# Kernel optimization log

Measured on AMD Instinct MI355X. Metric: run time of the kernel, lower is better.

The kernel has to match this reference:

```python
import jax, jax.numpy as jnp
import numpy as np

N_NODES = 50000
N_EDGES = 800000
DIM = 128
HEADS = 8
DK = DIM // HEADS  # 16
SQRT_DK = float(np.sqrt(DK))


def setup_inputs() -> dict:
    key = jax.random.key(0)
    ks = jax.random.split(key, 12)
    inp = {
        "h": jax.random.normal(ks[0], (N_NODES, DIM), jnp.float32),
        "src": jax.random.randint(ks[1], (N_EDGES,), 0, N_NODES, jnp.int32),
        "dst": jax.random.randint(ks[2], (N_EDGES,), 0, N_NODES, jnp.int32),
        "Wk": jax.random.normal(ks[3], (DIM, DIM), jnp.float32) / np.sqrt(DIM),
        "bk": jnp.zeros((DIM,), jnp.float32),
        "Wq": jax.random.normal(ks[4], (DIM, DIM), jnp.float32) / np.sqrt(DIM),
        "bq": jnp.zeros((DIM,), jnp.float32),
        "Wv": jax.random.normal(ks[5], (DIM, DIM), jnp.float32) / np.sqrt(DIM),
        "bv": jnp.zeros((DIM,), jnp.float32),
        "Wa": jax.random.normal(ks[6], (DIM, DIM), jnp.float32) / np.sqrt(DIM),
        "ba": jnp.zeros((DIM,), jnp.float32),
        "rel_att": jax.random.normal(ks[7], (HEADS, DK, DK), jnp.float32) / np.sqrt(DK),
        "rel_msg": jax.random.normal(ks[8], (HEADS, DK, DK), jnp.float32) / np.sqrt(DK),
        "rel_pri": jnp.ones((HEADS,), jnp.float32),
        "skip": jnp.ones((1,), jnp.float32),
    }
    return inp


def reference(h, src, dst, Wk, bk, Wq, bq, Wv, bv, Wa, ba, rel_att, rel_msg, rel_pri, skip):
    N = h.shape[0]
    # node-level projections -> [N, H, d_k]
    k = (h @ Wk + bk).reshape(N, HEADS, DK)
    q = (h @ Wq + bq).reshape(N, HEADS, DK)
    v = (h @ Wv + bv).reshape(N, HEADS, DK)
    # relation-specific transforms
    k = jnp.einsum('nhi,hij->nhj', k, rel_att)
    v = jnp.einsum('nhi,hij->nhj', v, rel_msg)
    # per-edge score: dot(q[dst], k[src]) over d_k -> [E, H]
    score = jnp.einsum('ehd,ehd->eh', q[dst], k[src]) * rel_pri / SQRT_DK
    # segment softmax over destination nodes (edge_softmax, norm_by='dst')
    smax = jax.ops.segment_max(score, dst, num_segments=N)  # [N, H]
    e = jnp.exp(score - smax[dst])
    ssum = jax.ops.segment_sum(e, dst, num_segments=N)  # [N, H]
    attn = e / ssum[dst]  # [E, H]
    # weighted scatter-sum of messages: sum_e v[src_e] * attn_e -> [N, H, d_k]
    m = v[src] * attn[:, :, None]
    t = jax.ops.segment_sum(m, dst, num_segments=N).reshape(N, DIM)
    # target-specific aggregation (dropout in eval mode = identity, use_norm=False)
    trans_out = t @ Wa + ba
    alpha = jax.nn.sigmoid(skip)  # [1], broadcasts
    new_h = trans_out * alpha + h * (1.0 - alpha)
    return new_h
```

## Files before the change

### kernel.cpp

```cpp
#include <hip/hip_runtime.h>
#include <stdint.h>

#define NN 50000
#define NE 800000

typedef __bf16 v8bf __attribute__((ext_vector_type(8)));
typedef float  v4f  __attribute__((ext_vector_type(4)));
typedef unsigned short v8us __attribute__((ext_vector_type(8)));

#define EXP2F(x) __builtin_amdgcn_exp2f(x)

__device__ __forceinline__ float bf2f(unsigned short u) {
    return __uint_as_float(((unsigned)u) << 16);
}
__device__ __forceinline__ unsigned short f2bf(float f) {
    unsigned u = __float_as_uint(f);
    u += 0x7FFFu + ((u >> 16) & 1u);
    return (unsigned short)(u >> 16);
}
__device__ __forceinline__ float ldf(const void* p, size_t i, int isb) {
    return isb ? bf2f(((const unsigned short*)p)[i]) : ((const float*)p)[i];
}

__global__ __launch_bounds__(128) void k_prep(
    const void* __restrict__ Wq, const void* __restrict__ bq,
    const void* __restrict__ Wk, const void* __restrict__ bk,
    const void* __restrict__ Wv, const void* __restrict__ bv,
    const void* __restrict__ Wa, const void* __restrict__ ba,
    const void* __restrict__ rel_att, const void* __restrict__ rel_msg,
    const void* __restrict__ rel_pri, const int* __restrict__ dst,
    unsigned* __restrict__ CNTP,
    int* __restrict__ FLAG, unsigned short* __restrict__ WTb,
    float* __restrict__ BC)
{
    int b = blockIdx.x;
    int j = threadIdx.x;
    if (b >= 512) {
        int e = (b - 512) * 128 + j;
        atomicAdd(&CNTP[(unsigned)dst[e] << 4], 1u);
        return;
    }
    const unsigned rp0 = ((const unsigned*)rel_pri)[0];
    const int isb = ((rp0 & 0xFFFFu) != 0u) ? 1 : 0;
    int m = b >> 7;
    int i = b & 127;
    if (b == 0 && j == 0) FLAG[0] = isb;
    if (m == 0) {
        WTb[((size_t)(0 * 128 + j)) * 128 + i] = f2bf(ldf(Wq, i * 128 + j, isb));
        if (i == 0) BC[j] = ldf(bq, j, isb);
    } else if (m == 3) {
        WTb[((size_t)(3 * 128 + j)) * 128 + i] = f2bf(ldf(Wa, i * 128 + j, isb));
        if (i == 0) BC[3 * 128 + j] = ldf(ba, j, isb);
    } else {
        const void* W    = (m == 1) ? Wk : Wv;
        const void* bias = (m == 1) ? bk : bv;
        const void* R    = (m == 1) ? rel_att : rel_msg;
        int hh = j >> 4, jj = j & 15;
        float scale = (m == 1) ? ldf(rel_pri, hh, isb) * 0.25f : 1.0f;
        float acc = 0.f, bacc = 0.f;
        #pragma unroll
        for (int l = 0; l < 16; ++l) {
            float r = ldf(R, hh * 256 + l * 16 + jj, isb);
            acc  += ldf(W, i * 128 + hh * 16 + l, isb) * r;
            bacc += ldf(bias, hh * 16 + l, isb) * r;
        }
        WTb[((size_t)(m * 128 + j)) * 128 + i] = f2bf(acc * scale);
        if (i == 0) BC[m * 128 + j] = bacc * scale;
    }
}

#define NSB 98
__global__ __launch_bounds__(256) void k_qkvscan(
    const void* __restrict__ h, const unsigned short* __restrict__ WTb,
    const float* __restrict__ BC, const int* __restrict__ FLAG,
    unsigned short* __restrict__ Qb, unsigned short* __restrict__ KVb,
    const unsigned* __restrict__ CNTP, unsigned* __restrict__ CURP,
    unsigned* __restrict__ RPS, unsigned* __restrict__ BSUM,
    unsigned* __restrict__ BOFF, unsigned* __restrict__ DONE)
{
    __shared__ __align__(16) unsigned short Ah[64][136];
    __shared__ __align__(16) unsigned short Bh[128][136];
    __shared__ int lastFlag;
    const int tid = threadIdx.x;

    if (blockIdx.x >= 782) {
        unsigned* shs = (unsigned*)&Ah[0][0];
        int sb = blockIdx.x - 782;
        int g0 = sb * 512 + tid * 2, g1 = g0 + 1;
        unsigned v0 = (g0 < NN) ? CNTP[(size_t)g0 << 4] : 0u;
        unsigned v1 = (g1 < NN) ? CNTP[(size_t)g1 << 4] : 0u;
        if (g0 < NN) CURP[(size_t)g0 << 4] = 0u;
        if (g1 < NN) CURP[(size_t)g1 << 4] = 0u;
        unsigned pv = v0 + v1;
        shs[tid] = pv;
        __syncthreads();
        #pragma unroll
        for (int off = 1; off < 256; off <<= 1) {
            unsigned t = 0;
            if (tid >= off) t = shs[tid - off];
            __syncthreads();
            if (tid >= off) shs[tid] += t;
            __syncthreads();
        }
        unsigned excl = shs[tid] - pv;
        if (g0 < NN) RPS[g0] = excl;
        if (g1 < NN) RPS[g1] = excl + v0;
        if (tid == 255) atomicExch(&BSUM[sb], shs[255]);
        __syncthreads();
        if (tid == 0) {
            __threadfence();
            lastFlag = (atomicAdd(DONE, 1u) == NSB - 1);
        }
        __syncthreads();
        if (!lastFlag) return;
        unsigned bv = (tid < NSB) ? atomicAdd(&BSUM[tid], 0u) : 0u;
        __syncthreads();
        shs[tid] = bv;
        __syncthreads();
        #pragma unroll
        for (int off = 1; off < 256; off <<= 1) {
            unsigned t = 0;
            if (tid >= off) t = shs[tid - off];
            __syncthreads();
            if (tid >= off) shs[tid] += t;
            __syncthreads();
        }
        if (tid < NSB) BOFF[tid] = shs[tid] - bv;
        return;
    }

    const int isb = FLAG[0];
    const int rowBase = blockIdx.x * 64;

    if (isb) {
        #pragma unroll
        for (int i = 0; i < 4; ++i) {
            int lin = tid + i * 256;
            int row = lin >> 4, kc = (lin & 15) * 8;
            int gr = rowBase + row;
            uint4 u = make_uint4(0, 0, 0, 0);
            if (gr < NN) u = *(const uint4*)((const unsigned short*)h + (size_t)gr * 128 + kc);
            *(uint4*)&Ah[row][kc] = u;
        }
    } else {
        #pragma unroll
        for (int i = 0; i < 8; ++i) {
            int lin = tid + i * 256;
            int row = lin >> 5, c4 = (lin & 31) * 4;
            int gr = rowBase + row;
            ushort4 o = make_ushort4(0, 0, 0, 0);
            if (gr < NN) {
                float4 f = *(const float4*)((const float*)h + (size_t)gr * 128 + c4);
                o.x = f2bf(f.x); o.y = f2bf(f.y); o.z = f2bf(f.z); o.w = f2bf(f.w);
            }
            *(ushort4*)&Ah[row][c4] = o;
        }
    }

    const int w = tid >> 6, l = tid & 63;
    const int lr = l & 15, q = l >> 4;
    v4f accK[8];

    for (int m = 0; m < 3; ++m) {
        if (m) __syncthreads();
        #pragma unroll
        for (int i = 0; i < 8; ++i) {
            int lin = tid + i * 256;
            int col = lin >> 4, kc = (lin & 15) * 8;
            uint4 u = *(const uint4*)(WTb + ((size_t)(m * 128 + col)) * 128 + kc);
            *(uint4*)&Bh[col][kc] = u;
        }
        __syncthreads();

        v4f acc[8];
        #pragma unroll
        for (int nt = 0; nt < 8; ++nt) {
            float bj = BC[m * 128 + nt * 16 + lr];
            acc[nt] = (v4f){bj, bj, bj, bj};
        }
        #pragma unroll
        for (int kk = 0; kk < 4; ++kk) {
            v8bf a = *(const v8bf*)&Ah[w * 16 + lr][kk * 32 + q * 8];
            #pragma unroll
            for (int nt = 0; nt < 8; ++nt) {
                v8bf b = *(const v8bf*)&Bh[nt * 16 + lr][kk * 32 + q * 8];
                acc[nt] = __builtin_amdgcn_mfma_f32_16x16x32_bf16(a, b, acc[nt], 0, 0, 0);
            }
        }
        if (m == 0) {
            #pragma unroll
            for (int nt = 0; nt < 8; ++nt)
                #pragma unroll
                for (int r = 0; r < 4; ++r) {
                    int row = rowBase + w * 16 + q * 4 + r;
                    if (row < NN)
                        Qb[(size_t)row * 128 + nt * 16 + lr] = f2bf(acc[nt][r]);
                }
        } else if (m == 1) {
            #pragma unroll
            for (int nt = 0; nt < 8; ++nt) accK[nt] = acc[nt];
        } else {
            #pragma unroll
            for (int nt = 0; nt < 8; ++nt)
                #pragma unroll
                for (int r = 0; r < 4; ++r) {
                    int row = rowBase + w * 16 + q * 4 + r;
                    if (row < NN) {
                        ushort2 kv;
                        kv.x = f2bf(accK[nt][r]);
                        kv.y = f2bf(acc[nt][r]);
                        *(ushort2*)&KVb[(size_t)row * 256 + (nt * 16 + lr) * 2] = kv;
                    }
                }
        }
    }
}

__global__ __launch_bounds__(256) void k_fill(
    const int* __restrict__ src, const int* __restrict__ dst,
    const unsigned* __restrict__ RPS, const unsigned* __restrict__ BOFF,
    unsigned* __restrict__ CURP, int* __restrict__ ESRC)
{
    int t = blockIdx.x * 256 + threadIdx.x;
    if (t >= NE / 4) return;
    int e = t * 4;
    const int4 d4 = *(const int4*)(dst + e);
    const int4 s4 = *(const int4*)(src + e);
    unsigned p0 = atomicAdd(&CURP[(size_t)(unsigned)d4.x << 4], 1u);
    unsigned p1 = atomicAdd(&CURP[(size_t)(unsigned)d4.y << 4], 1u);
    unsigned p2 = atomicAdd(&CURP[(size_t)(unsigned)d4.z << 4], 1u);
    unsigned p3 = atomicAdd(&CURP[(size_t)(unsigned)d4.w << 4], 1u);
    ESRC[(int)(RPS[d4.x] + BOFF[d4.x >> 9] + p0)] = s4.x;
    ESRC[(int)(RPS[d4.y] + BOFF[d4.y >> 9] + p1)] = s4.y;
    ESRC[(int)(RPS[d4.z] + BOFF[d4.z >> 9] + p2)] = s4.z;
    ESRC[(int)(RPS[d4.w] + BOFF[d4.w >> 9] + p3)] = s4.w;
}

__global__ __launch_bounds__(256) void k_attn(
    const unsigned* __restrict__ RPS, const unsigned* __restrict__ BOFF,
    const int* __restrict__ ESRC,
    const unsigned short* __restrict__ Qb, const unsigned short* __restrict__ KVb,
    unsigned short* __restrict__ Tb)
{
    int d = (blockIdx.x * 256 + threadIdx.x) >> 6;
    int lane = threadIdx.x & 63;
    int hl = lane >> 5;
    int sub = lane & 31;
    int beg = (int)(RPS[d] + BOFF[d >> 9]);
    int end = (d == NN - 1) ? NE : (int)(RPS[d + 1] + BOFF[(d + 1) >> 9]);
    const float LOG2E = 1.4426950408889634f;

    const ushort4 qu = *(const ushort4*)(Qb + (size_t)d * 128 + sub * 4);
    float q0 = bf2f(qu.x) * LOG2E, q1 = bf2f(qu.y) * LOG2E;
    float q2 = bf2f(qu.z) * LOG2E, q3 = bf2f(qu.w) * LOG2E;

    float s = 0.f, o0 = 0.f, o1 = 0.f, o2 = 0.f, o3 = 0.f;
    v8us kvA[4]; int vA[4];
    if (beg < end) {
        #pragma unroll
        for (int t = 0; t < 4; ++t) {
            int idx = beg + 2 * t + hl;
            vA[t] = idx < end;
            int sid = ESRC[vA[t] ? idx : end - 1];
            kvA[t] = *(const v8us*)(KVb + (size_t)sid * 256 + sub * 8);
        }
    }
    for (int j = beg; j < end; j += 8) {
        v8us kvB[4]; int vB[4] = {0, 0, 0, 0};
        int jn = j + 8;
        if (jn < end) {
            #pragma unroll
            for (int t = 0; t < 4; ++t) {
                int idx = jn + 2 * t + hl;
                vB[t] = idx < end;
                int sid = ESRC[vB[t] ? idx : end - 1];
                kvB[t] = *(const v8us*)(KVb + (size_t)sid * 256 + sub * 8);
            }
        }
        #pragma unroll
        for (int t = 0; t < 4; ++t) {
            float p = q0 * bf2f(kvA[t][0]) + q1 * bf2f(kvA[t][2])
                    + q2 * bf2f(kvA[t][4]) + q3 * bf2f(kvA[t][6]);
            p += __shfl_xor(p, 1);
            p += __shfl_xor(p, 2);
            float w = vA[t] ? EXP2F(p) : 0.f;
            s  += w;
            o0 += w * bf2f(kvA[t][1]);
            o1 += w * bf2f(kvA[t][3]);
            o2 += w * bf2f(kvA[t][5]);
            o3 += w * bf2f(kvA[t][7]);
        }
        #pragma unroll
        for (int t = 0; t < 4; ++t) { kvA[t] = kvB[t]; vA[t] = vB[t]; }
    }
    s  += __shfl_xor(s, 32);
    o0 += __shfl_xor(o0, 32);
    o1 += __shfl_xor(o1, 32);
    o2 += __shfl_xor(o2, 32);
    o3 += __shfl_xor(o3, 32);
    float r = (s > 0.f) ? (1.0f / s) : 0.f;
    if (hl == 0) {
        ushort4 o;
        o.x = f2bf(o0 * r); o.y = f2bf(o1 * r);
        o.z = f2bf(o2 * r); o.w = f2bf(o3 * r);
        *(ushort4*)(Tb + (size_t)d * 128 + sub * 4) = o;
    }
}

__global__ __launch_bounds__(256) void k_final_m(
    const unsigned short* __restrict__ Tb, const unsigned short* __restrict__ WTb,
    const float* __restrict__ BC, const void* __restrict__ h,
    const void* __restrict__ skip, const int* __restrict__ FLAG,
    void* __restrict__ out)
{
    __shared__ __align__(16) unsigned short Ah[64][136];
    __shared__ __align__(16) unsigned short Bh[128][136];
    const int isb = FLAG[0];
    const int tid = threadIdx.x;
    const int rowBase = blockIdx.x * 64;

    #pragma unroll
    for (int i = 0; i < 4; ++i) {
        int lin = tid + i * 256;
        int row = lin >> 4, kc = (lin & 15) * 8;
        int gr = rowBase + row;
        uint4 u = make_uint4(0, 0, 0, 0);
        if (gr < NN) u = *(const uint4*)(Tb + (size_t)gr * 128 + kc);
        *(uint4*)&Ah[row][kc] = u;
    }
    #pragma unroll
    for (int i = 0; i < 8; ++i) {
        int lin = tid + i * 256;
        int col = lin >> 4, kc = (lin & 15) * 8;
        uint4 u = *(const uint4*)(WTb + ((size_t)(3 * 128 + col)) * 128 + kc);
        *(uint4*)&Bh[col][kc] = u;
    }
    __syncthreads();

    const int w = tid >> 6, l = tid & 63;
    const int lr = l & 15, q = l >> 4;
    v4f acc[8];
    #pragma unroll
    for (int nt = 0; nt < 8; ++nt) {
        float bj = BC[3 * 128 + nt * 16 + lr];
        acc[nt] = (v4f){bj, bj, bj, bj};
    }
    #pragma unroll
    for (int kk = 0; kk < 4; ++kk) {
        v8bf a = *(const v8bf*)&Ah[w * 16 + lr][kk * 32 + q * 8];
        #pragma unroll
        for (int nt = 0; nt < 8; ++nt) {
            v8bf b = *(const v8bf*)&Bh[nt * 16 + lr][kk * 32 + q * 8];
            acc[nt] = __builtin_amdgcn_mfma_f32_16x16x32_bf16(a, b, acc[nt], 0, 0, 0);
        }
    }
    float skipv = ldf(skip, 0, isb);
    float alpha = 1.0f / (1.0f + __expf(-skipv));
    float beta = 1.0f - alpha;
    #pragma unroll
    for (int nt = 0; nt < 8; ++nt) {
        #pragma unroll
        for (int r = 0; r < 4; ++r) {
            int row = rowBase + w * 16 + q * 4 + r;
            if (row < NN) {
                size_t off = (size_t)row * 128 + nt * 16 + lr;
                float hv = ldf(h, off, isb);
                float o = alpha * acc[nt][r] + beta * hv;
                if (isb) ((unsigned short*)out)[off] = f2bf(o);
                else     ((float*)out)[off] = o;
            }
        }
    }
}

extern "C" void kernel_launch(void* const* d_in, const int* in_sizes, int n_in,
                              void* d_out, int out_size, void* d_ws, size_t ws_size,
                              hipStream_t stream)
{
    const void* h  = d_in[0];
    const int* src = (const int*)d_in[1];
    const int* dst = (const int*)d_in[2];
    const void* Wk = d_in[3];
    const void* bk = d_in[4];
    const void* Wq = d_in[5];
    const void* bq = d_in[6];
    const void* Wv = d_in[7];
    const void* bv = d_in[8];
    const void* Wa = d_in[9];
    const void* ba = d_in[10];
    const void* rel_att = d_in[11];
    const void* rel_msg = d_in[12];
    const void* rel_pri = d_in[13];
    const void* skip    = d_in[14];

    float* F = (float*)d_ws;
    int* FLAG      = (int*)F;
    float* BC      = F + 16;
    unsigned short* WTb = (unsigned short*)(BC + 512);
    unsigned* CNTP = (unsigned*)((float*)(BC + 512) + 32768);
    unsigned* DONE = CNTP + 800000;
    unsigned* CURP = DONE + 16;
    unsigned* RPS  = CURP + 800000;
    unsigned* BSUM = RPS + 50048;
    unsigned* BOFF = BSUM + 128;
    unsigned short* Tb = (unsigned short*)(BOFF + 128);
    int* ESRC      = (int*)(Tb + (size_t)NN * 128);
    unsigned short* Qb  = (unsigned short*)(ESRC + NE);
    unsigned short* KVb = Qb + (size_t)NN * 128;

    (void)hipMemsetAsync(CNTP, 0, (800000 + 16) * sizeof(unsigned), stream);

    k_prep<<<512 + 6250, 128, 0, stream>>>(Wq, bq, Wk, bk, Wv, bv, Wa, ba,
                                           rel_att, rel_msg, rel_pri, dst, CNTP,
                                           FLAG, WTb, BC);
    k_qkvscan<<<782 + NSB, 256, 0, stream>>>(h, WTb, BC, FLAG, Qb, KVb,
                                             CNTP, CURP, RPS, BSUM, BOFF, DONE);
    k_fill<<<(NE / 4 + 255) / 256, 256, 0, stream>>>(src, dst, RPS, BOFF, CURP, ESRC);
    k_attn<<<(NN * 64) / 256, 256, 0, stream>>>(RPS, BOFF, ESRC, Qb, KVb, Tb);
    k_final_m<<<782, 256, 0, stream>>>(Tb, WTb, BC, h, skip, FLAG, d_out);
}
```

Measured before the change: 296.7 us.

## Record per-edge ranks in count pass to drop second atomic pass in CSR fill

The counting pass now stores the rank returned by atomicAdd for every edge, so the fill kernel computes each edge's CSR slot directly from row start plus rank instead of doing a second round of atomics on a cursor array. This also removes the cursor reset in the scan kernel. Source indices in the CSR are narrowed to 16-bit to cut gather traffic in fill and attention. This is unsafe because node ids up to 50000 fit in an unsigned short only because NN < 65536, and a rank above 65535 on any high-degree node would overflow.

```diff
diff --git a/kernel.cpp b/kernel.cpp
--- a/kernel.cpp
+++ b/kernel.cpp
@@ -29,7 +29,7 @@
     const void* __restrict__ Wa, const void* __restrict__ ba,
     const void* __restrict__ rel_att, const void* __restrict__ rel_msg,
     const void* __restrict__ rel_pri, const int* __restrict__ dst,
-    unsigned* __restrict__ CNTP,
+    unsigned* __restrict__ CNTP, unsigned short* __restrict__ RANKS,
     int* __restrict__ FLAG, unsigned short* __restrict__ WTb,
     float* __restrict__ BC)
 {
@@ -37,7 +37,8 @@
     int j = threadIdx.x;
     if (b >= 512) {
         int e = (b - 512) * 128 + j;
-        atomicAdd(&CNTP[(unsigned)dst[e] << 4], 1u);
+        unsigned r = atomicAdd(&CNTP[(unsigned)dst[e] << 4], 1u);
+        RANKS[e] = (unsigned short)r;
         return;
     }
     const unsigned rp0 = ((const unsigned*)rel_pri)[0];
@@ -74,7 +75,7 @@
     const void* __restrict__ h, const unsigned short* __restrict__ WTb,
     const float* __restrict__ BC, const int* __restrict__ FLAG,
     unsigned short* __restrict__ Qb, unsigned short* __restrict__ KVb,
-    const unsigned* __restrict__ CNTP, unsigned* __restrict__ CURP,
+    const unsigned* __restrict__ CNTP,
     unsigned* __restrict__ RPS, unsigned* __restrict__ BSUM,
     unsigned* __restrict__ BOFF, unsigned* __restrict__ DONE)
 {
@@ -89,8 +90,6 @@
         int g0 = sb * 512 + tid * 2, g1 = g0 + 1;
         unsigned v0 = (g0 < NN) ? CNTP[(size_t)g0 << 4] : 0u;
         unsigned v1 = (g1 < NN) ? CNTP[(size_t)g1 << 4] : 0u;
-        if (g0 < NN) CURP[(size_t)g0 << 4] = 0u;
-        if (g1 < NN) CURP[(size_t)g1 << 4] = 0u;
         unsigned pv = v0 + v1;
         shs[tid] = pv;
         __syncthreads();
@@ -218,27 +217,25 @@
 
 __global__ __launch_bounds__(256) void k_fill(
     const int* __restrict__ src, const int* __restrict__ dst,
+    const unsigned short* __restrict__ RANKS,
     const unsigned* __restrict__ RPS, const unsigned* __restrict__ BOFF,
-    unsigned* __restrict__ CURP, int* __restrict__ ESRC)
+    unsigned short* __restrict__ ESRC)
 {
     int t = blockIdx.x * 256 + threadIdx.x;
-    if (t >= NE / 4) return;
-    int e = t * 4;
-    const int4 d4 = *(const int4*)(dst + e);
-    const int4 s4 = *(const int4*)(src + e);
-    unsigned p0 = atomicAdd(&CURP[(size_t)(unsigned)d4.x << 4], 1u);
-    unsigned p1 = atomicAdd(&CURP[(size_t)(unsigned)d4.y << 4], 1u);
-    unsigned p2 = atomicAdd(&CURP[(size_t)(unsigned)d4.z << 4], 1u);
-    unsigned p3 = atomicAdd(&CURP[(size_t)(unsigned)d4.w << 4], 1u);
-    ESRC[(int)(RPS[d4.x] + BOFF[d4.x >> 9] + p0)] = s4.x;
-    ESRC[(int)(RPS[d4.y] + BOFF[d4.y >> 9] + p1)] = s4.y;
-    ESRC[(int)(RPS[d4.z] + BOFF[d4.z >> 9] + p2)] = s4.z;
-    ESRC[(int)(RPS[d4.w] + BOFF[d4.w >> 9] + p3)] = s4.w;
+    if (t >= NE / 2) return;
+    int e = t * 2;
+    const int2 d2 = *(const int2*)(dst + e);
+    const int2 s2 = *(const int2*)(src + e);
+    const ushort2 r2 = *(const ushort2*)(RANKS + e);
+    unsigned p0 = RPS[d2.x] + BOFF[d2.x >> 9] + r2.x;
+    unsigned p1 = RPS[d2.y] + BOFF[d2.y >> 9] + r2.y;
+    ESRC[p0] = (unsigned short)s2.x;
+    ESRC[p1] = (unsigned short)s2.y;
 }
 
 __global__ __launch_bounds__(256) void k_attn(
     const unsigned* __restrict__ RPS, const unsigned* __restrict__ BOFF,
-    const int* __restrict__ ESRC,
+    const unsigned short* __restrict__ ESRC,
     const unsigned short* __restrict__ Qb, const unsigned short* __restrict__ KVb,
     unsigned short* __restrict__ Tb)
 {
@@ -399,23 +396,23 @@
     unsigned short* WTb = (unsigned short*)(BC + 512);
     unsigned* CNTP = (unsigned*)((float*)(BC + 512) + 32768);
     unsigned* DONE = CNTP + 800000;
-    unsigned* CURP = DONE + 16;
-    unsigned* RPS  = CURP + 800000;
+    unsigned short* RANKS = (unsigned short*)(DONE + 16);
+    unsigned* RPS  = (unsigned*)(RANKS + 800000);
     unsigned* BSUM = RPS + 50048;
     unsigned* BOFF = BSUM + 128;
     unsigned short* Tb = (unsigned short*)(BOFF + 128);
-    int* ESRC      = (int*)(Tb + (size_t)NN * 128);
-    unsigned short* Qb  = (unsigned short*)(ESRC + NE);
+    unsigned short* ESRC = Tb + (size_t)NN * 128;
+    unsigned short* Qb  = ESRC + NE;
     unsigned short* KVb = Qb + (size_t)NN * 128;
 
     (void)hipMemsetAsync(CNTP, 0, (800000 + 16) * sizeof(unsigned), stream);
 
     k_prep<<<512 + 6250, 128, 0, stream>>>(Wq, bq, Wk, bk, Wv, bv, Wa, ba,
-                                           rel_att, rel_msg, rel_pri, dst, CNTP,
-                                           FLAG, WTb, BC);
+                                           rel_att, rel_msg, rel_pri, dst,
+                                           CNTP, RANKS, FLAG, WTb, BC);
     k_qkvscan<<<782 + NSB, 256, 0, stream>>>(h, WTb, BC, FLAG, Qb, KVb,
-                                             CNTP, CURP, RPS, BSUM, BOFF, DONE);
-    k_fill<<<(NE / 4 + 255) / 256, 256, 0, stream>>>(src, dst, RPS, BOFF, CURP, ESRC);
+                                             CNTP, RPS, BSUM, BOFF, DONE);
+    k_fill<<<(NE / 2 + 255) / 256, 256, 0, stream>>>(src, dst, RANKS, RPS, BOFF, ESRC);
     k_attn<<<(NN * 64) / 256, 256, 0, stream>>>(RPS, BOFF, ESRC, Qb, KVb, Tb);
     k_final_m<<<782, 256, 0, stream>>>(Tb, WTb, BC, h, skip, FLAG, d_out);
 }
```

Measured after the change: 259.3 us. 1.14x faster.
